# Kernel tuning notes

Measured on AMD Instinct MI355X. Metric: run time of the kernel, lower is better.

## Reference

```python
import jax, jax.numpy as jnp
import numpy as np

D = 256        # n_unit
H = 2          # n_head
FF = 256       # n_hid
WIN = 99       # N-1 in source: row i attends to cols [i-99, i]
NEG = -1e30    # additive mask value (-inf in torch)
LN_EPS = 1e-5


def _layer_norm(x, w, b):
    mu = jnp.mean(x, axis=-1, keepdims=True)
    var = jnp.mean((x - mu) ** 2, axis=-1, keepdims=True)
    return (x - mu) * jax.lax.rsqrt(var + LN_EPS) * w + b


def _pos_encoding(S, d):
    pos = jnp.arange(S, dtype=jnp.float32)[:, None]                      # [S,1]
    div = jnp.exp(jnp.arange(0, d, 2, dtype=jnp.float32) * (-np.log(10000.0) / d))
    ang = pos * div                                                      # [S,d/2]
    return jnp.stack([jnp.sin(ang), jnp.cos(ang)], axis=-1).reshape(S, d)


def _band_mask(S):
    i = jnp.arange(S)[:, None]
    j = jnp.arange(S)[None, :]
    allowed = (j <= i) & (j >= i - WIN)
    return jnp.where(allowed, 0.0, NEG).astype(jnp.float32)             # [S,S]


def setup_inputs() -> dict:
    key = jax.random.key(0)
    ks = jax.random.split(key, 24)
    B, S, IN = 8, 2000, 256
    s = 0.02
    inp = {
        "src": jax.random.normal(ks[0], (B, S, IN), jnp.float32),
        "input_lengths": jax.random.randint(ks[1], (B,), 1, S + 1).astype(jnp.int64),
        # encoder Linear(in_size, n_unit); torch Linear weight is [out,in]
        "W_enc": jax.random.normal(ks[2], (D, IN), jnp.float32) * s,
        "b_enc": jnp.zeros((D,), jnp.float32),
        # MHA packed qkv projection
        "in_proj_w": jax.random.normal(ks[3], (3 * D, D), jnp.float32) * s,
        "in_proj_b": jnp.zeros((3 * D,), jnp.float32),
        "out_proj_w": jax.random.normal(ks[4], (D, D), jnp.float32) * s,
        "out_proj_b": jnp.zeros((D,), jnp.float32),
        "ln1_w": jnp.ones((D,), jnp.float32),
        "ln1_b": jnp.zeros((D,), jnp.float32),
        # FFN
        "lin1_w": jax.random.normal(ks[5], (FF, D), jnp.float32) * s,
        "lin1_b": jnp.zeros((FF,), jnp.float32),
        "lin2_w": jax.random.normal(ks[6], (D, FF), jnp.float32) * s,
        "lin2_b": jnp.zeros((D,), jnp.float32),
        "ln2_w": jnp.ones((D,), jnp.float32),
        "ln2_b": jnp.zeros((D,), jnp.float32),
        # output head
        "fc1_w": jax.random.normal(ks[7], (D // 4, D), jnp.float32) * s,
        "fc1_b": jnp.zeros((D // 4,), jnp.float32),
        "fc2_w": jax.random.normal(ks[8], (1, D // 4), jnp.float32) * s,
        "fc2_b": jnp.zeros((1,), jnp.float32),
    }
    return inp


def reference(src, input_lengths, W_enc, b_enc, in_proj_w, in_proj_b,
              out_proj_w, out_proj_b, ln1_w, ln1_b, lin1_w, lin1_b,
              lin2_w, lin2_b, ln2_w, ln2_b, fc1_w, fc1_b, fc2_w, fc2_b):
    B, S, _ = src.shape
    hd = D // H
    # input projection + positional encoding (dropout is identity at eval)
    x = src @ W_enc.T + b_enc                                            # [B,S,D]
    x = x + _pos_encoding(S, D)[None]
    # --- TransformerEncoderLayer (post-norm, relu) with banded causal mask ---
    qkv = x @ in_proj_w.T + in_proj_b                                    # [B,S,3D]
    q, k, v = jnp.split(qkv, 3, axis=-1)
    q = q.reshape(B, S, H, hd)
    k = k.reshape(B, S, H, hd)
    v = v.reshape(B, S, H, hd)
    scores = jnp.einsum('bihd,bjhd->bhij', q, k) / np.sqrt(hd)           # [B,H,S,S]
    scores = scores + _band_mask(S)[None, None]
    attn = jax.nn.softmax(scores, axis=-1)
    ctx = jnp.einsum('bhij,bjhd->bihd', attn, v).reshape(B, S, D)
    attn_out = ctx @ out_proj_w.T + out_proj_b
    x = _layer_norm(x + attn_out, ln1_w, ln1_b)
    ff = jax.nn.relu(x @ lin1_w.T + lin1_b) @ lin2_w.T + lin2_b
    x = _layer_norm(x + ff, ln2_w, ln2_b)
    # --- output head (no activation between fc1 and fc2, per source) ---
    out = x @ fc1_w.T + fc1_b                                            # [B,S,D/4]
    logits = out @ fc2_w.T + fc2_b                                       # [B,S,1]
    return logits.reshape(B, -1)                                         # [B,S]
```

## Files before the change

### kernel.cpp

```cpp
#include <hip/hip_runtime.h>
#include <math.h>

#define SLEN 2000
#define BATCH 8
#define MTOK 16000
#define WIN 99

typedef __attribute__((ext_vector_type(8))) short short8;
typedef __attribute__((ext_vector_type(4))) float floatx4;

__device__ __forceinline__ float bf2f(unsigned int h) {
  union { unsigned int u; float f; } w; w.u = h << 16; return w.f;
}
__device__ __forceinline__ unsigned short f2bf(float f) {
  union { float f; unsigned int u; } w; w.f = f;
  return (unsigned short)((w.u + 0x7fffu + ((w.u >> 16) & 1u)) >> 16);
}

typedef const __attribute__((address_space(1))) unsigned int* gas_t;
typedef __attribute__((address_space(3))) unsigned int* las_t;
__device__ __forceinline__ void gload_lds16(const unsigned short* g, unsigned short* l) {
  __builtin_amdgcn_global_load_lds((gas_t)g, (las_t)l, 16, 0, 0);
}

__device__ __forceinline__ void cvt4(const float* __restrict__ in,
                                     unsigned short* __restrict__ out, int i) {
  float4 v = ((const float4*)in)[i];
  ushort4 o;
  o.x = f2bf(v.x); o.y = f2bf(v.y); o.z = f2bf(v.z); o.w = f2bf(v.w);
  ((ushort4*)out)[i] = o;
}

__global__ __launch_bounds__(256) void k_prep(
    const float* __restrict__ wenc,     unsigned short* __restrict__ wencb,
    const float* __restrict__ wqk,      unsigned short* __restrict__ wqkb,
    const float* __restrict__ wout,     unsigned short* __restrict__ woutb,
    const float* __restrict__ wl1,      unsigned short* __restrict__ wl1b,
    const float* __restrict__ wl2,      unsigned short* __restrict__ wl2b,
    float* __restrict__ pe,
    const float* __restrict__ fc1w, const float* __restrict__ fc1b,
    const float* __restrict__ fc2w, const float* __restrict__ fc2b,
    const float* __restrict__ ln2w, const float* __restrict__ ln2b,
    float* __restrict__ hp) {
  __shared__ float red0[4], red1[4];
  const int bx = blockIdx.x, tid = threadIdx.x;
  if (bx < 64)         { cvt4(wenc, wencb, bx * 256 + tid); }
  else if (bx < 256)   { cvt4(wqk,  wqkb,  (bx - 64) * 256 + tid); }
  else if (bx < 320)   { cvt4(wout, woutb, (bx - 256) * 256 + tid); }
  else if (bx < 384)   { cvt4(wl1,  wl1b,  (bx - 320) * 256 + tid); }
  else if (bx < 448)   { cvt4(wl2,  wl2b,  (bx - 384) * 256 + tid); }
  else if (bx < 948) {
    int i4 = (bx - 448) * 256 + tid;
    int e0 = i4 * 4;
    int s  = e0 >> 8;
    int d0 = e0 & 255;
    float dv0 = expf((float)(d0 >> 1) * -0.07195578415606394f);
    float dv1 = expf((float)((d0 >> 1) + 1) * -0.07195578415606394f);
    float a0 = (float)s * dv0, a1 = (float)s * dv1;
    float4 o = make_float4(sinf(a0), cosf(a0), sinf(a1), cosf(a1));
    ((float4*)pe)[i4] = o;
  } else {
    int k = tid;
    float we = 0.f;
#pragma unroll 8
    for (int o = 0; o < 64; ++o) we += fc2w[o] * fc1w[o * 256 + k];
    float c1 = ln2w[k] * we;
    hp[k] = c1;
    float p0 = ln2b[k] * we;
    if (k < 64) p0 += fc2w[k] * fc1b[k];
    float s0 = p0, s1 = c1;
#pragma unroll
    for (int off = 32; off; off >>= 1) {
      s0 += __shfl_xor(s0, off);
      s1 += __shfl_xor(s1, off);
    }
    int wv = k >> 6;
    if ((k & 63) == 0) { red0[wv] = s0; red1[wv] = s1; }
    __syncthreads();
    if (k == 0) {
      hp[256] = red0[0] + red0[1] + red0[2] + red0[3] + fc2b[0];
      hp[257] = red1[0] + red1[1] + red1[2] + red1[3];
    }
  }
}

#define XPAD 264

__global__ __launch_bounds__(256) void k_pre(
    const float* __restrict__ src,
    const unsigned short* __restrict__ wenc, const float* __restrict__ benc,
    const float* __restrict__ pe,
    const unsigned short* __restrict__ wqk, const float* __restrict__ bqk,
    unsigned short* __restrict__ xb, unsigned short* __restrict__ qkvb) {
  __shared__ __align__(16) unsigned short Xt[64 * XPAD];
  __shared__ __align__(16) unsigned short Achk[64 * 32];
  __shared__ __align__(16) unsigned short Bchk[256 * 32];
  const int tid = threadIdx.x, lane = tid & 63, w = tid >> 6;
  const int m0 = blockIdx.x * 64;
  const int yy = blockIdx.y;
  const int plo = yy ? 1 : 0;
  const int phi = yy ? 3 : 1;
  const int kq = lane >> 4, ml = lane & 15;
  const int myrow = w * 16 + ml;
  const int cq = lane >> 4, cl = lane & 15;

  const int ar = tid >> 2, as = tid & 3;
  const int ac = as ^ ((ar >> 1) & 3);
  const float* asrc = src + (size_t)(m0 + ar) * 256 + ac * 8;

  int brow[4], bsc[4];
#pragma unroll
  for (int i = 0; i < 4; ++i) {
    brow[i] = (w * 4 + i) * 16 + (lane >> 2);
    bsc[i]  = (lane & 3) ^ ((brow[i] >> 1) & 3);
  }

  floatx4 acc[16] = {};
  for (int kt = 0; kt < 256; kt += 32) {
    __syncthreads();
    {
      float4 v0 = *(const float4*)(asrc + kt);
      float4 v1 = *(const float4*)(asrc + kt + 4);
      unsigned short t8[8] = {f2bf(v0.x), f2bf(v0.y), f2bf(v0.z), f2bf(v0.w),
                              f2bf(v1.x), f2bf(v1.y), f2bf(v1.z), f2bf(v1.w)};
      *(uint4*)&Achk[ar * 32 + as * 8] = *(const uint4*)t8;
    }
#pragma unroll
    for (int i = 0; i < 4; ++i)
      gload_lds16(wenc + (size_t)brow[i] * 256 + kt + bsc[i] * 8, &Bchk[(w * 4 + i) * 512]);
    __syncthreads();

    int sa = kq ^ ((myrow >> 1) & 3);
    short8 af = *(const short8*)&Achk[myrow * 32 + sa * 8];
#pragma unroll
    for (int nt = 0; nt < 16; ++nt) {
      int n = nt * 16 + ml;
      int sb = kq ^ ((n >> 1) & 3);
      short8 bf = *(const short8*)&Bchk[n * 32 + sb * 8];
      acc[nt] = __builtin_amdgcn_mfma_f32_16x16x32_bf16(af, bf, acc[nt], 0, 0, 0);
    }
  }
#pragma unroll
  for (int nt = 0; nt < 16; ++nt) {
#pragma unroll
    for (int r = 0; r < 4; ++r) {
      int lrow = w * 16 + cq * 4 + r;
      int row  = m0 + lrow;
      int col  = nt * 16 + cl;
      float v = acc[nt][r] + benc[col] + pe[(size_t)(row % SLEN) * 256 + col];
      unsigned short hv = f2bf(v);
      Xt[lrow * XPAD + col] = hv;
      if (yy == 0) xb[(size_t)row * 256 + col] = hv;
    }
  }

  for (int p = plo; p < phi; ++p) {
    floatx4 a2[16] = {};
    for (int kt = 0; kt < 256; kt += 32) {
      __syncthreads();
#pragma unroll
      for (int i = 0; i < 4; ++i)
        gload_lds16(wqk + (size_t)(p * 256 + brow[i]) * 256 + kt + bsc[i] * 8,
                    &Bchk[(w * 4 + i) * 512]);
      __syncthreads();
      short8 af = *(const short8*)&Xt[myrow * XPAD + kt + kq * 8];
#pragma unroll
      for (int nt = 0; nt < 16; ++nt) {
        int n = nt * 16 + ml;
        int sb = kq ^ ((n >> 1) & 3);
        short8 bf = *(const short8*)&Bchk[n * 32 + sb * 8];
        a2[nt] = __builtin_amdgcn_mfma_f32_16x16x32_bf16(af, bf, a2[nt], 0, 0, 0);
      }
    }
#pragma unroll
    for (int nt = 0; nt < 16; ++nt) {
#pragma unroll
      for (int r = 0; r < 4; ++r) {
        int row = m0 + w * 16 + cq * 4 + r;
        int cg  = p * 256 + nt * 16 + cl;
        qkvb[(size_t)row * 768 + cg] = f2bf(a2[nt][r] + bqk[cg]);
      }
    }
  }
}

#define KPAD 136
#define VPAD 184
#define PPAD 132
#define UNION 176

__global__ __launch_bounds__(256) void k_attn_mfma(const unsigned short* __restrict__ qkv,
                                                   unsigned short* __restrict__ ctx) {
  __shared__ __align__(16) unsigned short KV[UNION * KPAD];
  __shared__ __align__(16) unsigned short Ps[4][16 * PPAD];
  const int tid  = threadIdx.x;
  const int lane = tid & 63;
  const int w    = tid >> 6;
  const int i0   = blockIdx.x * 64;
  const int b    = blockIdx.y;
  const int h    = blockIdx.z;
  const int jmin_u = i0 - WIN;
  const float scale = 0.08838834764831845f;

  const int qrow = i0 + w * 16 + (lane & 15);
  const unsigned short* qptr =
      qkv + (size_t)(b * SLEN + min(qrow, SLEN - 1)) * 768 + h * 128 + (lane >> 4) * 8;
  short8 qf[4];
#pragma unroll
  for (int kc = 0; kc < 4; ++kc) qf[kc] = *(const short8*)(qptr + kc * 32);

  for (int it = 0; it < 11; ++it) {
    int idx = it * 256 + tid;
    int row = idx >> 4;
    int c8  = idx & 15;
    int j = jmin_u + row;
    uint4 v = make_uint4(0u, 0u, 0u, 0u);
    if (j >= 0 && j < SLEN)
      v = *(const uint4*)(qkv + (size_t)(b * SLEN + j) * 768 + 256 + h * 128 + c8 * 8);
    *(uint4*)&KV[row * KPAD + c8 * 8] = v;
  }
  __syncthreads();

  const int koff = w * 16;
  floatx4 sc[8] = {};
#pragma unroll
  for (int kt = 0; kt < 8; ++kt) {
#pragma unroll
    for (int kc = 0; kc < 4; ++kc) {
      short8 kf = *(const short8*)&KV[(koff + kt * 16 + (lane & 15)) * KPAD
                                      + kc * 32 + (lane >> 4) * 8];
      sc[kt] = __builtin_amdgcn_mfma_f32_16x16x32_bf16(qf[kc], kf, sc[kt], 0, 0, 0);
    }
  }

  const int qme = i0 + w * 16 + (lane >> 4) * 4;
  const int jme = jmin_u + koff + (lane & 15);
  float mx[4] = {-1e30f, -1e30f, -1e30f, -1e30f};
#pragma unroll
  for (int kt = 0; kt < 8; ++kt) {
#pragma unroll
    for (int r = 0; r < 4; ++r) {
      int j = jme + kt * 16, q = qme + r;
      bool ok = (j >= 0) && (j >= q - WIN) && (j <= q);
      float s = ok ? sc[kt][r] : -1e30f;
      sc[kt][r] = s;
      mx[r] = fmaxf(mx[r], s);
    }
  }
#pragma unroll
  for (int r = 0; r < 4; ++r)
#pragma unroll
    for (int off = 8; off; off >>= 1) mx[r] = fmaxf(mx[r], __shfl_xor(mx[r], off, 16));

  float sum[4] = {0.f, 0.f, 0.f, 0.f};
#pragma unroll
  for (int kt = 0; kt < 8; ++kt)
#pragma unroll
    for (int r = 0; r < 4; ++r) {
      float e = __expf((sc[kt][r] - mx[r]) * scale);
      sc[kt][r] = e;
      sum[r] += e;
    }
#pragma unroll
  for (int r = 0; r < 4; ++r)
#pragma unroll
    for (int off = 8; off; off >>= 1) sum[r] += __shfl_xor(sum[r], off, 16);
  float rinv[4];
#pragma unroll
  for (int r = 0; r < 4; ++r) rinv[r] = 1.f / sum[r];

  unsigned short* pw = &Ps[w][0];
#pragma unroll
  for (int kt = 0; kt < 8; ++kt)
#pragma unroll
    for (int r = 0; r < 4; ++r)
      pw[((lane >> 4) * 4 + r) * PPAD + kt * 16 + (lane & 15)] = f2bf(sc[kt][r]);
  __syncthreads();

  for (int it = 0; it < 12; ++it) {
    int idx = it * 256 + tid;
    int grp = idx >> 6;
    int key = (grp >> 4) * 64 + (idx & 63);
    int c8  = grp & 15;
    if (key < UNION) {
      int j = jmin_u + key;
      uint4 v = make_uint4(0u, 0u, 0u, 0u);
      if (j >= 0 && j < SLEN)
        v = *(const uint4*)(qkv + (size_t)(b * SLEN + j) * 768 + 512 + h * 128 + c8 * 8);
      unsigned short e[8];
      *(uint4*)e = v;
      int d0 = c8 * 8;
#pragma unroll
      for (int i = 0; i < 8; ++i) KV[(d0 + i) * VPAD + key] = e[i];
    }
  }
  __syncthreads();

  floatx4 ov[8] = {};
#pragma unroll
  for (int kc = 0; kc < 4; ++kc) {
    short8 pf = *(const short8*)&pw[(lane & 15) * PPAD + kc * 32 + (lane >> 4) * 8];
#pragma unroll
    for (int dt = 0; dt < 8; ++dt) {
      short8 vf = *(const short8*)&KV[(dt * 16 + (lane & 15)) * VPAD
                                      + koff + kc * 32 + (lane >> 4) * 8];
      ov[dt] = __builtin_amdgcn_mfma_f32_16x16x32_bf16(pf, vf, ov[dt], 0, 0, 0);
    }
  }

#pragma unroll
  for (int dt = 0; dt < 8; ++dt)
#pragma unroll
    for (int r = 0; r < 4; ++r) {
      int q = qme + r;
      if (q < SLEN)
        ctx[(size_t)(b * SLEN + q) * 256 + h * 128 + dt * 16 + (lane & 15)] =
            f2bf(ov[dt][r] * rinv[r]);
    }
}

__global__ __launch_bounds__(256) void k_post(
    const unsigned short* __restrict__ ctx,
    const unsigned short* __restrict__ wout, const float* __restrict__ bout,
    const unsigned short* __restrict__ xb,
    const float* __restrict__ ln1w, const float* __restrict__ ln1b,
    const unsigned short* __restrict__ w1, const float* __restrict__ b1,
    const unsigned short* __restrict__ w2, const float* __restrict__ b2,
    const float* __restrict__ hp, float* __restrict__ out) {
  __shared__ __align__(16) unsigned short X1[64 * XPAD];
  __shared__ __align__(16) unsigned short Achk[64 * 32];
  __shared__ __align__(16) unsigned short Bchk[256 * 32];
  __shared__ float lnp[512];
  __shared__ float c1s[256];
  const int tid = threadIdx.x, lane = tid & 63, w = tid >> 6;
  const int m0 = blockIdx.x * 64;
  const int kq = lane >> 4, ml = lane & 15;
  const int myrow = w * 16 + ml;
  const int cq = lane >> 4, cl = lane & 15;

  lnp[tid] = ln1w[tid];
  lnp[256 + tid] = ln1b[tid];
  c1s[tid] = hp[tid];
  const float c0 = hp[256], sc1 = hp[257];

  int brow[4], bsc[4];
#pragma unroll
  for (int i = 0; i < 4; ++i) {
    brow[i] = (w * 4 + i) * 16 + (lane >> 2);
    bsc[i]  = (lane & 3) ^ ((brow[i] >> 1) & 3);
  }
  const int arow = w * 16 + (lane >> 2);
  const int asc  = (lane & 3) ^ ((arow >> 1) & 3);
  const unsigned short* actx = ctx + (size_t)(m0 + arow) * 256 + asc * 8;

  floatx4 acc[16] = {};
  for (int kt = 0; kt < 256; kt += 32) {
    __syncthreads();
    gload_lds16(actx + kt, &Achk[w * 512]);
#pragma unroll
    for (int i = 0; i < 4; ++i)
      gload_lds16(wout + (size_t)brow[i] * 256 + kt + bsc[i] * 8, &Bchk[(w * 4 + i) * 512]);
    __syncthreads();
    int sa = kq ^ ((myrow >> 1) & 3);
    short8 af = *(const short8*)&Achk[myrow * 32 + sa * 8];
#pragma unroll
    for (int nt = 0; nt < 16; ++nt) {
      int n = nt * 16 + ml;
      int sb = kq ^ ((n >> 1) & 3);
      short8 bf = *(const short8*)&Bchk[n * 32 + sb * 8];
      acc[nt] = __builtin_amdgcn_mfma_f32_16x16x32_bf16(af, bf, acc[nt], 0, 0, 0);
    }
  }
  float s_[4] = {0.f, 0.f, 0.f, 0.f}, q_[4] = {0.f, 0.f, 0.f, 0.f};
#pragma unroll
  for (int nt = 0; nt < 16; ++nt) {
#pragma unroll
    for (int r = 0; r < 4; ++r) {
      int row = m0 + w * 16 + cq * 4 + r;
      int col = nt * 16 + cl;
      float v = acc[nt][r] + bout[col] + bf2f(xb[(size_t)row * 256 + col]);
      acc[nt][r] = v;
      s_[r] += v;
      q_[r] += v * v;
    }
  }
#pragma unroll
  for (int r = 0; r < 4; ++r)
#pragma unroll
    for (int off = 8; off; off >>= 1) {
      s_[r] += __shfl_xor(s_[r], off, 16);
      q_[r] += __shfl_xor(q_[r], off, 16);
    }
  floatx4 x1sav[16];
#pragma unroll
  for (int r = 0; r < 4; ++r) {
    float mu  = s_[r] * (1.f / 256.f);
    float var = q_[r] * (1.f / 256.f) - mu * mu;
    float rr  = rsqrtf(var + 1e-5f);
    int lrow  = w * 16 + cq * 4 + r;
#pragma unroll
    for (int nt = 0; nt < 16; ++nt) {
      int col = nt * 16 + cl;
      float x1 = (acc[nt][r] - mu) * rr * lnp[col] + lnp[256 + col];
      x1sav[nt][r] = x1;
      X1[lrow * XPAD + col] = f2bf(x1);
    }
  }

#pragma unroll
  for (int nt = 0; nt < 16; ++nt) acc[nt] = (floatx4){0.f, 0.f, 0.f, 0.f};
  for (int kt = 0; kt < 256; kt += 32) {
    __syncthreads();
#pragma unroll
    for (int i = 0; i < 4; ++i)
      gload_lds16(w1 + (size_t)brow[i] * 256 + kt + bsc[i] * 8, &Bchk[(w * 4 + i) * 512]);
    __syncthreads();
    short8 af = *(const short8*)&X1[myrow * XPAD + kt + kq * 8];
#pragma unroll
    for (int nt = 0; nt < 16; ++nt) {
      int n = nt * 16 + ml;
      int sb = kq ^ ((n >> 1) & 3);
      short8 bf = *(const short8*)&Bchk[n * 32 + sb * 8];
      acc[nt] = __builtin_amdgcn_mfma_f32_16x16x32_bf16(af, bf, acc[nt], 0, 0, 0);
    }
  }
  __syncthreads();
#pragma unroll
  for (int nt = 0; nt < 16; ++nt) {
#pragma unroll
    for (int r = 0; r < 4; ++r) {
      int lrow = w * 16 + cq * 4 + r;
      int col  = nt * 16 + cl;
      X1[lrow * XPAD + col] = f2bf(fmaxf(acc[nt][r] + b1[col], 0.f));
    }
  }
  __syncthreads();

#pragma unroll
  for (int nt = 0; nt < 16; ++nt) acc[nt] = (floatx4){0.f, 0.f, 0.f, 0.f};
  for (int kt = 0; kt < 256; kt += 32) {
    __syncthreads();
#pragma unroll
    for (int i = 0; i < 4; ++i)
      gload_lds16(w2 + (size_t)brow[i] * 256 + kt + bsc[i] * 8, &Bchk[(w * 4 + i) * 512]);
    __syncthreads();
    short8 af = *(const short8*)&X1[myrow * XPAD + kt + kq * 8];
#pragma unroll
    for (int nt = 0; nt < 16; ++nt) {
      int n = nt * 16 + ml;
      int sb = kq ^ ((n >> 1) & 3);
      short8 bf = *(const short8*)&Bchk[n * 32 + sb * 8];
      acc[nt] = __builtin_amdgcn_mfma_f32_16x16x32_bf16(af, bf, acc[nt], 0, 0, 0);
    }
  }
  float ss[4] = {0.f, 0.f, 0.f, 0.f}, qq[4] = {0.f, 0.f, 0.f, 0.f}, dd[4] = {0.f, 0.f, 0.f, 0.f};
#pragma unroll
  for (int nt = 0; nt < 16; ++nt) {
#pragma unroll
    for (int r = 0; r < 4; ++r) {
      int col = nt * 16 + cl;
      float v = acc[nt][r] + b2[col] + x1sav[nt][r];
      ss[r] += v;
      qq[r] += v * v;
      dd[r] += v * c1s[col];
    }
  }
#pragma unroll
  for (int r = 0; r < 4; ++r)
#pragma unroll
    for (int off = 8; off; off >>= 1) {
      ss[r] += __shfl_xor(ss[r], off, 16);
      qq[r] += __shfl_xor(qq[r], off, 16);
      dd[r] += __shfl_xor(dd[r], off, 16);
    }
  if (cl == 0) {
#pragma unroll
    for (int r = 0; r < 4; ++r) {
      float mu  = ss[r] * (1.f / 256.f);
      float var = qq[r] * (1.f / 256.f) - mu * mu;
      float rr  = rsqrtf(var + 1e-5f);
      out[m0 + w * 16 + cq * 4 + r] = rr * (dd[r] - mu * sc1) + c0;
    }
  }
}

extern "C" void kernel_launch(void* const* d_in, const int* in_sizes, int n_in,
                              void* d_out, int out_size, void* d_ws, size_t ws_size,
                              hipStream_t stream) {
  const float* src        = (const float*)d_in[0];
  const float* W_enc      = (const float*)d_in[2];
  const float* b_enc      = (const float*)d_in[3];
  const float* in_proj_w  = (const float*)d_in[4];
  const float* in_proj_b  = (const float*)d_in[5];
  const float* out_proj_w = (const float*)d_in[6];
  const float* out_proj_b = (const float*)d_in[7];
  const float* ln1_w      = (const float*)d_in[8];
  const float* ln1_b      = (const float*)d_in[9];
  const float* lin1_w     = (const float*)d_in[10];
  const float* lin1_b     = (const float*)d_in[11];
  const float* lin2_w     = (const float*)d_in[12];
  const float* lin2_b     = (const float*)d_in[13];
  const float* ln2_w      = (const float*)d_in[14];
  const float* ln2_b      = (const float*)d_in[15];
  const float* fc1_w      = (const float*)d_in[16];
  const float* fc1_b      = (const float*)d_in[17];
  const float* fc2_w      = (const float*)d_in[18];
  const float* fc2_b      = (const float*)d_in[19];

  char* p = (char*)d_ws;
  float* pe            = (float*)p;           p += (size_t)SLEN * 256 * 4;
  float* hp            = (float*)p;           p += 2048;
  unsigned short* xb   = (unsigned short*)p;  p += (size_t)MTOK * 256 * 2;
  unsigned short* qkvb = (unsigned short*)p;  p += (size_t)MTOK * 768 * 2;
  unsigned short* ctxb = (unsigned short*)p;  p += (size_t)MTOK * 256 * 2;
  unsigned short* wencb= (unsigned short*)p;  p += 256 * 256 * 2;
  unsigned short* wqkb = (unsigned short*)p;  p += 768 * 256 * 2;
  unsigned short* woutb= (unsigned short*)p;  p += 256 * 256 * 2;
  unsigned short* wl1b = (unsigned short*)p;  p += 256 * 256 * 2;
  unsigned short* wl2b = (unsigned short*)p;  p += 256 * 256 * 2;

  k_prep<<<949, 256, 0, stream>>>(W_enc, wencb, in_proj_w, wqkb,
                                  out_proj_w, woutb, lin1_w, wl1b, lin2_w, wl2b,
                                  pe, fc1_w, fc1_b, fc2_w, fc2_b, ln2_w, ln2_b, hp);
  k_pre<<<dim3(MTOK / 64, 2), 256, 0, stream>>>(src, wencb, b_enc, pe, wqkb, in_proj_b, xb, qkvb);
  k_attn_mfma<<<dim3((SLEN + 63) / 64, BATCH, 2), 256, 0, stream>>>(qkvb, ctxb);
  k_post<<<MTOK / 64, 256, 0, stream>>>(ctxb, woutb, out_proj_b, xb, ln1_w, ln1_b,
                                        wl1b, lin1_b, wl2b, lin2_b, hp, (float*)d_out);
}
```

Before: 181.9 us.

## Re-tile pre/post GEMMs per-wave column slices with double-buffered weight staging

```diff
diff --git a/kernel.cpp b/kernel.cpp
--- a/kernel.cpp
+++ b/kernel.cpp
@@ -5,9 +5,13 @@
 #define BATCH 8
 #define MTOK 16000
 #define WIN 99
+#define XPAD 264
 
 typedef __attribute__((ext_vector_type(8))) short short8;
 typedef __attribute__((ext_vector_type(4))) float floatx4;
+
+#define WAITVM0() __builtin_amdgcn_s_waitcnt(0x0F70)
+#define WAITVM4() __builtin_amdgcn_s_waitcnt(0x0F74)
 
 __device__ __forceinline__ float bf2f(unsigned int h) {
   union { unsigned int u; float f; } w; w.u = h << 16; return w.f;
@@ -57,8 +61,7 @@
     float dv0 = expf((float)(d0 >> 1) * -0.07195578415606394f);
     float dv1 = expf((float)((d0 >> 1) + 1) * -0.07195578415606394f);
     float a0 = (float)s * dv0, a1 = (float)s * dv1;
-    float4 o = make_float4(sinf(a0), cosf(a0), sinf(a1), cosf(a1));
-    ((float4*)pe)[i4] = o;
+    ((float4*)pe)[i4] = make_float4(sinf(a0), cosf(a0), sinf(a1), cosf(a1));
   } else {
     int k = tid;
     float we = 0.f;
@@ -84,8 +87,6 @@
   }
 }
 
-#define XPAD 264
-
 __global__ __launch_bounds__(256) void k_pre(
     const float* __restrict__ src,
     const unsigned short* __restrict__ wenc, const float* __restrict__ benc,
@@ -93,94 +94,115 @@
     const unsigned short* __restrict__ wqk, const float* __restrict__ bqk,
     unsigned short* __restrict__ xb, unsigned short* __restrict__ qkvb) {
   __shared__ __align__(16) unsigned short Xt[64 * XPAD];
-  __shared__ __align__(16) unsigned short Achk[64 * 32];
-  __shared__ __align__(16) unsigned short Bchk[256 * 32];
+  __shared__ __align__(16) unsigned short Bst[4][2][2048];
   const int tid = threadIdx.x, lane = tid & 63, w = tid >> 6;
   const int m0 = blockIdx.x * 64;
-  const int yy = blockIdx.y;
-  const int plo = yy ? 1 : 0;
-  const int phi = yy ? 3 : 1;
   const int kq = lane >> 4, ml = lane & 15;
-  const int myrow = w * 16 + ml;
-  const int cq = lane >> 4, cl = lane & 15;
-
-  const int ar = tid >> 2, as = tid & 3;
-  const int ac = as ^ ((ar >> 1) & 3);
-  const float* asrc = src + (size_t)(m0 + ar) * 256 + ac * 8;
-
-  int brow[4], bsc[4];
+  const int wcolg = w * 64;
+
+  int grow[4], gsc[4];
 #pragma unroll
   for (int i = 0; i < 4; ++i) {
-    brow[i] = (w * 4 + i) * 16 + (lane >> 2);
-    bsc[i]  = (lane & 3) ^ ((brow[i] >> 1) & 3);
-  }
-
-  floatx4 acc[16] = {};
-  for (int kt = 0; kt < 256; kt += 32) {
-    __syncthreads();
-    {
-      float4 v0 = *(const float4*)(asrc + kt);
-      float4 v1 = *(const float4*)(asrc + kt + 4);
+    grow[i] = i * 16 + (lane >> 2);
+    gsc[i]  = (lane & 3) ^ ((grow[i] >> 1) & 3);
+  }
+
+  auto issueB = [&](const unsigned short* W, int kt, int buf) {
+#pragma unroll
+    for (int i = 0; i < 4; ++i)
+      gload_lds16(W + (size_t)(wcolg + grow[i]) * 256 + kt + gsc[i] * 8,
+                  &Bst[w][buf][i * 512]);
+  };
+  auto readB = [&](int buf, int nt) -> short8 {
+    int n = nt * 16 + ml;
+    int sb = kq ^ ((n >> 1) & 3);
+    return *(const short8*)&Bst[w][buf][n * 32 + sb * 8];
+  };
+
+  floatx4 acc[4][4] = {};
+#pragma unroll
+  for (int k8 = 0; k8 < 8; ++k8) {
+    const int kt = k8 * 32;
+    issueB(wenc, kt, k8 & 1);
+    short8 af[4];
+#pragma unroll
+    for (int mt = 0; mt < 4; ++mt) {
+      const float* ap = src + (size_t)(m0 + mt * 16 + ml) * 256 + kt + kq * 8;
+      float4 v0 = *(const float4*)ap;
+      float4 v1 = *(const float4*)(ap + 4);
       unsigned short t8[8] = {f2bf(v0.x), f2bf(v0.y), f2bf(v0.z), f2bf(v0.w),
                               f2bf(v1.x), f2bf(v1.y), f2bf(v1.z), f2bf(v1.w)};
-      *(uint4*)&Achk[ar * 32 + as * 8] = *(const uint4*)t8;
-    }
-#pragma unroll
-    for (int i = 0; i < 4; ++i)
-      gload_lds16(wenc + (size_t)brow[i] * 256 + kt + bsc[i] * 8, &Bchk[(w * 4 + i) * 512]);
-    __syncthreads();
-
-    int sa = kq ^ ((myrow >> 1) & 3);
-    short8 af = *(const short8*)&Achk[myrow * 32 + sa * 8];
-#pragma unroll
-    for (int nt = 0; nt < 16; ++nt) {
-      int n = nt * 16 + ml;
-      int sb = kq ^ ((n >> 1) & 3);
-      short8 bf = *(const short8*)&Bchk[n * 32 + sb * 8];
-      acc[nt] = __builtin_amdgcn_mfma_f32_16x16x32_bf16(af, bf, acc[nt], 0, 0, 0);
-    }
-  }
-#pragma unroll
-  for (int nt = 0; nt < 16; ++nt) {
-#pragma unroll
-    for (int r = 0; r < 4; ++r) {
-      int lrow = w * 16 + cq * 4 + r;
-      int row  = m0 + lrow;
-      int col  = nt * 16 + cl;
-      float v = acc[nt][r] + benc[col] + pe[(size_t)(row % SLEN) * 256 + col];
-      unsigned short hv = f2bf(v);
-      Xt[lrow * XPAD + col] = hv;
-      if (yy == 0) xb[(size_t)row * 256 + col] = hv;
-    }
-  }
-
-  for (int p = plo; p < phi; ++p) {
-    floatx4 a2[16] = {};
-    for (int kt = 0; kt < 256; kt += 32) {
-      __syncthreads();
-#pragma unroll
-      for (int i = 0; i < 4; ++i)
-        gload_lds16(wqk + (size_t)(p * 256 + brow[i]) * 256 + kt + bsc[i] * 8,
-                    &Bchk[(w * 4 + i) * 512]);
-      __syncthreads();
-      short8 af = *(const short8*)&Xt[myrow * XPAD + kt + kq * 8];
-#pragma unroll
-      for (int nt = 0; nt < 16; ++nt) {
-        int n = nt * 16 + ml;
-        int sb = kq ^ ((n >> 1) & 3);
-        short8 bf = *(const short8*)&Bchk[n * 32 + sb * 8];
-        a2[nt] = __builtin_amdgcn_mfma_f32_16x16x32_bf16(af, bf, a2[nt], 0, 0, 0);
-      }
-    }
-#pragma unroll
-    for (int nt = 0; nt < 16; ++nt) {
+      af[mt] = *(const short8*)t8;
+    }
+    WAITVM0();
+#pragma unroll
+    for (int nt = 0; nt < 4; ++nt) {
+      short8 bf = readB(k8 & 1, nt);
+#pragma unroll
+      for (int mt = 0; mt < 4; ++mt)
+        acc[mt][nt] = __builtin_amdgcn_mfma_f32_16x16x32_bf16(af[mt], bf, acc[mt][nt], 0, 0, 0);
+    }
+  }
+#pragma unroll
+  for (int mt = 0; mt < 4; ++mt)
+#pragma unroll
+    for (int nt = 0; nt < 4; ++nt)
 #pragma unroll
       for (int r = 0; r < 4; ++r) {
-        int row = m0 + w * 16 + cq * 4 + r;
-        int cg  = p * 256 + nt * 16 + cl;
-        qkvb[(size_t)row * 768 + cg] = f2bf(a2[nt][r] + bqk[cg]);
-      }
-    }
+        int lrow = mt * 16 + kq * 4 + r;
+        int col  = wcolg + nt * 16 + ml;
+        float v = acc[mt][nt][r] + benc[col]
+                + pe[(size_t)((m0 + lrow) % SLEN) * 256 + col];
+        unsigned short hv = f2bf(v);
+        Xt[lrow * XPAD + col] = hv;
+        xb[(size_t)(m0 + lrow) * 256 + col] = hv;
+      }
+  __syncthreads();
+
+  for (int p = 0; p < 3; ++p) {
+    const unsigned short* Wp = wqk + (size_t)p * 65536;
+    floatx4 a2[4][4] = {};
+    issueB(Wp, 0, 0);
+#pragma unroll
+    for (int k8 = 0; k8 < 7; ++k8) {
+      issueB(Wp, (k8 + 1) * 32, (k8 + 1) & 1);
+      WAITVM4();
+      short8 af[4];
+#pragma unroll
+      for (int mt = 0; mt < 4; ++mt)
+        af[mt] = *(const short8*)&Xt[(mt * 16 + ml) * XPAD + k8 * 32 + kq * 8];
+#pragma unroll
+      for (int nt = 0; nt < 4; ++nt) {
+        short8 bf = readB(k8 & 1, nt);
+#pragma unroll
+        for (int mt = 0; mt < 4; ++mt)
+          a2[mt][nt] = __builtin_amdgcn_mfma_f32_16x16x32_bf16(af[mt], bf, a2[mt][nt], 0, 0, 0);
+      }
+    }
+    WAITVM0();
+    {
+      short8 af[4];
+#pragma unroll
+      for (int mt = 0; mt < 4; ++mt)
+        af[mt] = *(const short8*)&Xt[(mt * 16 + ml) * XPAD + 224 + kq * 8];
+#pragma unroll
+      for (int nt = 0; nt < 4; ++nt) {
+        short8 bf = readB(1, nt);
+#pragma unroll
+        for (int mt = 0; mt < 4; ++mt)
+          a2[mt][nt] = __builtin_amdgcn_mfma_f32_16x16x32_bf16(af[mt], bf, a2[mt][nt], 0, 0, 0);
+      }
+    }
+#pragma unroll
+    for (int mt = 0; mt < 4; ++mt)
+#pragma unroll
+      for (int nt = 0; nt < 4; ++nt)
+#pragma unroll
+        for (int r = 0; r < 4; ++r) {
+          int row = m0 + mt * 16 + kq * 4 + r;
+          int cg  = p * 256 + wcolg + nt * 16 + ml;
+          qkvb[(size_t)row * 768 + cg] = f2bf(a2[mt][nt][r] + bqk[cg]);
+        }
   }
 }
 
@@ -328,159 +350,244 @@
     const unsigned short* __restrict__ w2, const float* __restrict__ b2,
     const float* __restrict__ hp, float* __restrict__ out) {
   __shared__ __align__(16) unsigned short X1[64 * XPAD];
-  __shared__ __align__(16) unsigned short Achk[64 * 32];
-  __shared__ __align__(16) unsigned short Bchk[256 * 32];
+  __shared__ __align__(16) unsigned short Bst[4][2][2048];
+  __shared__ float lnred[4][64][3];
+  __shared__ float lnstat[64][2];
   __shared__ float lnp[512];
   __shared__ float c1s[256];
   const int tid = threadIdx.x, lane = tid & 63, w = tid >> 6;
   const int m0 = blockIdx.x * 64;
   const int kq = lane >> 4, ml = lane & 15;
-  const int myrow = w * 16 + ml;
-  const int cq = lane >> 4, cl = lane & 15;
+  const int wcolg = w * 64;
 
   lnp[tid] = ln1w[tid];
   lnp[256 + tid] = ln1b[tid];
   c1s[tid] = hp[tid];
-  const float c0 = hp[256], sc1 = hp[257];
-
-  int brow[4], bsc[4];
+  const float c0h = hp[256], sc1 = hp[257];
+
+  int grow[4], gsc[4];
 #pragma unroll
   for (int i = 0; i < 4; ++i) {
-    brow[i] = (w * 4 + i) * 16 + (lane >> 2);
-    bsc[i]  = (lane & 3) ^ ((brow[i] >> 1) & 3);
-  }
-  const int arow = w * 16 + (lane >> 2);
-  const int asc  = (lane & 3) ^ ((arow >> 1) & 3);
-  const unsigned short* actx = ctx + (size_t)(m0 + arow) * 256 + asc * 8;
-
-  floatx4 acc[16] = {};
-  for (int kt = 0; kt < 256; kt += 32) {
-    __syncthreads();
-    gload_lds16(actx + kt, &Achk[w * 512]);
+    grow[i] = i * 16 + (lane >> 2);
+    gsc[i]  = (lane & 3) ^ ((grow[i] >> 1) & 3);
+  }
+  auto issueB = [&](const unsigned short* W, int kt, int buf) {
 #pragma unroll
     for (int i = 0; i < 4; ++i)
-      gload_lds16(wout + (size_t)brow[i] * 256 + kt + bsc[i] * 8, &Bchk[(w * 4 + i) * 512]);
-    __syncthreads();
-    int sa = kq ^ ((myrow >> 1) & 3);
-    short8 af = *(const short8*)&Achk[myrow * 32 + sa * 8];
-#pragma unroll
-    for (int nt = 0; nt < 16; ++nt) {
-      int n = nt * 16 + ml;
-      int sb = kq ^ ((n >> 1) & 3);
-      short8 bf = *(const short8*)&Bchk[n * 32 + sb * 8];
-      acc[nt] = __builtin_amdgcn_mfma_f32_16x16x32_bf16(af, bf, acc[nt], 0, 0, 0);
-    }
-  }
-  float s_[4] = {0.f, 0.f, 0.f, 0.f}, q_[4] = {0.f, 0.f, 0.f, 0.f};
-#pragma unroll
-  for (int nt = 0; nt < 16; ++nt) {
+      gload_lds16(W + (size_t)(wcolg + grow[i]) * 256 + kt + gsc[i] * 8,
+                  &Bst[w][buf][i * 512]);
+  };
+  auto readB = [&](int buf, int nt) -> short8 {
+    int n = nt * 16 + ml;
+    int sb = kq ^ ((n >> 1) & 3);
+    return *(const short8*)&Bst[w][buf][n * 32 + sb * 8];
+  };
+
+  floatx4 acc[4][4] = {};
+#pragma unroll
+  for (int k8 = 0; k8 < 8; ++k8) {
+    const int kt = k8 * 32;
+    issueB(wout, kt, k8 & 1);
+    short8 af[4];
+#pragma unroll
+    for (int mt = 0; mt < 4; ++mt)
+      af[mt] = *(const short8*)(ctx + (size_t)(m0 + mt * 16 + ml) * 256 + kt + kq * 8);
+    WAITVM0();
+#pragma unroll
+    for (int nt = 0; nt < 4; ++nt) {
+      short8 bf = readB(k8 & 1, nt);
+#pragma unroll
+      for (int mt = 0; mt < 4; ++mt)
+        acc[mt][nt] = __builtin_amdgcn_mfma_f32_16x16x32_bf16(af[mt], bf, acc[mt][nt], 0, 0, 0);
+    }
+  }
+  float s_[4][4], q_[4][4];
+#pragma unroll
+  for (int mt = 0; mt < 4; ++mt)
+#pragma unroll
+    for (int r = 0; r < 4; ++r) { s_[mt][r] = 0.f; q_[mt][r] = 0.f; }
+#pragma unroll
+  for (int mt = 0; mt < 4; ++mt)
+#pragma unroll
+    for (int nt = 0; nt < 4; ++nt)
+#pragma unroll
+      for (int r = 0; r < 4; ++r) {
+        int lrow = mt * 16 + kq * 4 + r;
+        int col  = wcolg + nt * 16 + ml;
+        float v = acc[mt][nt][r] + bout[col]
+                + bf2f(xb[(size_t)(m0 + lrow) * 256 + col]);
+        acc[mt][nt][r] = v;
+        s_[mt][r] += v;
+        q_[mt][r] += v * v;
+      }
+#pragma unroll
+  for (int mt = 0; mt < 4; ++mt)
 #pragma unroll
     for (int r = 0; r < 4; ++r) {
-      int row = m0 + w * 16 + cq * 4 + r;
-      int col = nt * 16 + cl;
-      float v = acc[nt][r] + bout[col] + bf2f(xb[(size_t)row * 256 + col]);
-      acc[nt][r] = v;
-      s_[r] += v;
-      q_[r] += v * v;
-    }
-  }
-#pragma unroll
-  for (int r = 0; r < 4; ++r)
-#pragma unroll
-    for (int off = 8; off; off >>= 1) {
-      s_[r] += __shfl_xor(s_[r], off, 16);
-      q_[r] += __shfl_xor(q_[r], off, 16);
-    }
-  floatx4 x1sav[16];
-#pragma unroll
-  for (int r = 0; r < 4; ++r) {
-    float mu  = s_[r] * (1.f / 256.f);
-    float var = q_[r] * (1.f / 256.f) - mu * mu;
+#pragma unroll
+      for (int off = 8; off; off >>= 1) {
+        s_[mt][r] += __shfl_xor(s_[mt][r], off, 16);
+        q_[mt][r] += __shfl_xor(q_[mt][r], off, 16);
+      }
+      if (ml == 0) {
+        int lrow = mt * 16 + kq * 4 + r;
+        lnred[w][lrow][0] = s_[mt][r];
+        lnred[w][lrow][1] = q_[mt][r];
+      }
+    }
+  __syncthreads();
+  if (tid < 64) {
+    float s = lnred[0][tid][0] + lnred[1][tid][0] + lnred[2][tid][0] + lnred[3][tid][0];
+    float q = lnred[0][tid][1] + lnred[1][tid][1] + lnred[2][tid][1] + lnred[3][tid][1];
+    float mu  = s * (1.f / 256.f);
+    float var = q * (1.f / 256.f) - mu * mu;
+    lnstat[tid][0] = mu;
+    lnstat[tid][1] = rsqrtf(var + 1e-5f);
+  }
+  __syncthreads();
+  floatx4 x1sav[4][4];
+#pragma unroll
+  for (int mt = 0; mt < 4; ++mt)
+#pragma unroll
+    for (int r = 0; r < 4; ++r) {
+      int lrow = mt * 16 + kq * 4 + r;
+      float mu = lnstat[lrow][0], rr = lnstat[lrow][1];
+#pragma unroll
+      for (int nt = 0; nt < 4; ++nt) {
+        int col = wcolg + nt * 16 + ml;
+        float x1 = (acc[mt][nt][r] - mu) * rr * lnp[col] + lnp[256 + col];
+        x1sav[mt][nt][r] = x1;
+        X1[lrow * XPAD + col] = f2bf(x1);
+      }
+    }
+  __syncthreads();
+
+#pragma unroll
+  for (int mt = 0; mt < 4; ++mt)
+#pragma unroll
+    for (int nt = 0; nt < 4; ++nt) acc[mt][nt] = (floatx4){0.f, 0.f, 0.f, 0.f};
+  issueB(w1, 0, 0);
+#pragma unroll
+  for (int k8 = 0; k8 < 7; ++k8) {
+    issueB(w1, (k8 + 1) * 32, (k8 + 1) & 1);
+    WAITVM4();
+    short8 af[4];
+#pragma unroll
+    for (int mt = 0; mt < 4; ++mt)
+      af[mt] = *(const short8*)&X1[(mt * 16 + ml) * XPAD + k8 * 32 + kq * 8];
+#pragma unroll
+    for (int nt = 0; nt < 4; ++nt) {
+      short8 bf = readB(k8 & 1, nt);
+#pragma unroll
+      for (int mt = 0; mt < 4; ++mt)
+        acc[mt][nt] = __builtin_amdgcn_mfma_f32_16x16x32_bf16(af[mt], bf, acc[mt][nt], 0, 0, 0);
+    }
+  }
+  WAITVM0();
+  {
+    short8 af[4];
+#pragma unroll
+    for (int mt = 0; mt < 4; ++mt)
+      af[mt] = *(const short8*)&X1[(mt * 16 + ml) * XPAD + 224 + kq * 8];
+#pragma unroll
+    for (int nt = 0; nt < 4; ++nt) {
+      short8 bf = readB(1, nt);
+#pragma unroll
+      for (int mt = 0; mt < 4; ++mt)
+        acc[mt][nt] = __builtin_amdgcn_mfma_f32_16x16x32_bf16(af[mt], bf, acc[mt][nt], 0, 0, 0);
+    }
+  }
+  __syncthreads();
+#pragma unroll
+  for (int mt = 0; mt < 4; ++mt)
+#pragma unroll
+    for (int nt = 0; nt < 4; ++nt)
+#pragma unroll
+      for (int r = 0; r < 4; ++r) {
+        int lrow = mt * 16 + kq * 4 + r;
+        int col  = wcolg + nt * 16 + ml;
+        X1[lrow * XPAD + col] = f2bf(fmaxf(acc[mt][nt][r] + b1[col], 0.f));
+      }
+  __syncthreads();
+
+#pragma unroll
+  for (int mt = 0; mt < 4; ++mt)
+#pragma unroll
+    for (int nt = 0; nt < 4; ++nt) acc[mt][nt] = (floatx4){0.f, 0.f, 0.f, 0.f};
+  issueB(w2, 0, 0);
+#pragma unroll
+  for (int k8 = 0; k8 < 7; ++k8) {
+    issueB(w2, (k8 + 1) * 32, (k8 + 1) & 1);
+    WAITVM4();
+    short8 af[4];
+#pragma unroll
+    for (int mt = 0; mt < 4; ++mt)
+      af[mt] = *(const short8*)&X1[(mt * 16 + ml) * XPAD + k8 * 32 + kq * 8];
+#pragma unroll
+    for (int nt = 0; nt < 4; ++nt) {
+      short8 bf = readB(k8 & 1, nt);
+#pragma unroll
+      for (int mt = 0; mt < 4; ++mt)
+        acc[mt][nt] = __builtin_amdgcn_mfma_f32_16x16x32_bf16(af[mt], bf, acc[mt][nt], 0, 0, 0);
+    }
+  }
+  WAITVM0();
+  {
+    short8 af[4];
+#pragma unroll
+    for (int mt = 0; mt < 4; ++mt)
+      af[mt] = *(const short8*)&X1[(mt * 16 + ml) * XPAD + 224 + kq * 8];
+#pragma unroll
+    for (int nt = 0; nt < 4; ++nt) {
+      short8 bf = readB(1, nt);
+#pragma unroll
+      for (int mt = 0; mt < 4; ++mt)
+        acc[mt][nt] = __builtin_amdgcn_mfma_f32_16x16x32_bf16(af[mt], bf, acc[mt][nt], 0, 0, 0);
+    }
+  }
+  float ss[4][4], qq[4][4], dd[4][4];
+#pragma unroll
+  for (int mt = 0; mt < 4; ++mt)
+#pragma unroll
+    for (int r = 0; r < 4; ++r) { ss[mt][r] = 0.f; qq[mt][r] = 0.f; dd[mt][r] = 0.f; }
+#pragma unroll
+  for (int mt = 0; mt < 4; ++mt)
+#pragma unroll
+    for (int nt = 0; nt < 4; ++nt)
+#pragma unroll
+      for (int r = 0; r < 4; ++r) {
+        int col = wcolg + nt * 16 + ml;
+        float v = acc[mt][nt][r] + b2[col] + x1sav[mt][nt][r];
+        ss[mt][r] += v;
+        qq[mt][r] += v * v;
+        dd[mt][r] += v * c1s[col];
+      }
+#pragma unroll
+  for (int mt = 0; mt < 4; ++mt)
+#pragma unroll
+    for (int r = 0; r < 4; ++r) {
+#pragma unroll
+      for (int off = 8; off; off >>= 1) {
+        ss[mt][r] += __shfl_xor(ss[mt][r], off, 16);
+        qq[mt][r] += __shfl_xor(qq[mt][r], off, 16);
+        dd[mt][r] += __shfl_xor(dd[mt][r], off, 16);
+      }
+      if (ml == 0) {
+        int lrow = mt * 16 + kq * 4 + r;
+        lnred[w][lrow][0] = ss[mt][r];
+        lnred[w][lrow][1] = qq[mt][r];
+        lnred[w][lrow][2] = dd[mt][r];
+      }
+    }
+  __syncthreads();
+  if (tid < 64) {
+    float s = lnred[0][tid][0] + lnred[1][tid][0] + lnred[2][tid][0] + lnred[3][tid][0];
+    float q = lnred[0][tid][1] + lnred[1][tid][1] + lnred[2][tid][1] + lnred[3][tid][1];
+    float d = lnred[0][tid][2] + lnred[1][tid][2] + lnred[2][tid][2] + lnred[3][tid][2];
+    float mu  = s * (1.f / 256.f);
+    float var = q * (1.f / 256.f) - mu * mu;
     float rr  = rsqrtf(var + 1e-5f);
-    int lrow  = w * 16 + cq * 4 + r;
-#pragma unroll
-    for (int nt = 0; nt < 16; ++nt) {
-      int col = nt * 16 + cl;
-      float x1 = (acc[nt][r] - mu) * rr * lnp[col] + lnp[256 + col];
-      x1sav[nt][r] = x1;
-      X1[lrow * XPAD + col] = f2bf(x1);
-    }
-  }
-
-#pragma unroll
-  for (int nt = 0; nt < 16; ++nt) acc[nt] = (floatx4){0.f, 0.f, 0.f, 0.f};
-  for (int kt = 0; kt < 256; kt += 32) {
-    __syncthreads();
-#pragma unroll
-    for (int i = 0; i < 4; ++i)
-      gload_lds16(w1 + (size_t)brow[i] * 256 + kt + bsc[i] * 8, &Bchk[(w * 4 + i) * 512]);
-    __syncthreads();
-    short8 af = *(const short8*)&X1[myrow * XPAD + kt + kq * 8];
-#pragma unroll
-    for (int nt = 0; nt < 16; ++nt) {
-      int n = nt * 16 + ml;
-      int sb = kq ^ ((n >> 1) & 3);
-      short8 bf = *(const short8*)&Bchk[n * 32 + sb * 8];
-      acc[nt] = __builtin_amdgcn_mfma_f32_16x16x32_bf16(af, bf, acc[nt], 0, 0, 0);
-    }
-  }
-  __syncthreads();
-#pragma unroll
-  for (int nt = 0; nt < 16; ++nt) {
-#pragma unroll
-    for (int r = 0; r < 4; ++r) {
-      int lrow = w * 16 + cq * 4 + r;
-      int col  = nt * 16 + cl;
-      X1[lrow * XPAD + col] = f2bf(fmaxf(acc[nt][r] + b1[col], 0.f));
-    }
-  }
-  __syncthreads();
-
-#pragma unroll
-  for (int nt = 0; nt < 16; ++nt) acc[nt] = (floatx4){0.f, 0.f, 0.f, 0.f};
-  for (int kt = 0; kt < 256; kt += 32) {
-    __syncthreads();
-#pragma unroll
-    for (int i = 0; i < 4; ++i)
-      gload_lds16(w2 + (size_t)brow[i] * 256 + kt + bsc[i] * 8, &Bchk[(w * 4 + i) * 512]);
-    __syncthreads();
-    short8 af = *(const short8*)&X1[myrow * XPAD + kt + kq * 8];
-#pragma unroll
-    for (int nt = 0; nt < 16; ++nt) {
-      int n = nt * 16 + ml;
-      int sb = kq ^ ((n >> 1) & 3);
-      short8 bf = *(const short8*)&Bchk[n * 32 + sb * 8];
-      acc[nt] = __builtin_amdgcn_mfma_f32_16x16x32_bf16(af, bf, acc[nt], 0, 0, 0);
-    }
-  }
-  float ss[4] = {0.f, 0.f, 0.f, 0.f}, qq[4] = {0.f, 0.f, 0.f, 0.f}, dd[4] = {0.f, 0.f, 0.f, 0.f};
-#pragma unroll
-  for (int nt = 0; nt < 16; ++nt) {
-#pragma unroll
-    for (int r = 0; r < 4; ++r) {
-      int col = nt * 16 + cl;
-      float v = acc[nt][r] + b2[col] + x1sav[nt][r];
-      ss[r] += v;
-      qq[r] += v * v;
-      dd[r] += v * c1s[col];
-    }
-  }
-#pragma unroll
-  for (int r = 0; r < 4; ++r)
-#pragma unroll
-    for (int off = 8; off; off >>= 1) {
-      ss[r] += __shfl_xor(ss[r], off, 16);
-      qq[r] += __shfl_xor(qq[r], off, 16);
-      dd[r] += __shfl_xor(dd[r], off, 16);
-    }
-  if (cl == 0) {
-#pragma unroll
-    for (int r = 0; r < 4; ++r) {
-      float mu  = ss[r] * (1.f / 256.f);
-      float var = qq[r] * (1.f / 256.f) - mu * mu;
-      float rr  = rsqrtf(var + 1e-5f);
-      out[m0 + w * 16 + cq * 4 + r] = rr * (dd[r] - mu * sc1) + c0;
-    }
+    out[m0 + tid] = rr * (d - mu * sc1) + c0h;
   }
 }
 
@@ -522,7 +629,7 @@
   k_prep<<<949, 256, 0, stream>>>(W_enc, wencb, in_proj_w, wqkb,
                                   out_proj_w, woutb, lin1_w, wl1b, lin2_w, wl2b,
                                   pe, fc1_w, fc1_b, fc2_w, fc2_b, ln2_w, ln2_b, hp);
-  k_pre<<<dim3(MTOK / 64, 2), 256, 0, stream>>>(src, wencb, b_enc, pe, wqkb, in_proj_b, xb, qkvb);
+  k_pre<<<MTOK / 64, 256, 0, stream>>>(src, wencb, b_enc, pe, wqkb, in_proj_b, xb, qkvb);
   k_attn_mfma<<<dim3((SLEN + 63) / 64, BATCH, 2), 256, 0, stream>>>(qkvb, ctxb);
   k_post<<<MTOK / 64, 256, 0, stream>>>(ctxb, woutb, out_proj_b, xb, ln1_w, ln1_b,
                                         wl1b, lin1_b, wl2b, lin2_b, hp, (float*)d_out);
```

New measurement: 173.5 us. -4.6%, faster.
